# Performance work log

Hardware: AMD Instinct MI355X
Metric: run time of the kernel (lower is better)

## Reference

```python
import jax, jax.numpy as jnp
import numpy as np


def _mlp2(x, W1, b1, W2, b2):
    # ReluMLP with two Dense layers: relu between layers, linear output
    return jax.nn.relu(x @ W1 + b1) @ W2 + b2


def setup_inputs() -> dict:
    key = jax.random.key(0)
    N, NP, DIN, D = 100000, 25000, 16, 64
    E, EDS, EP, EUS = 1_600_000, 800_000, 400_000, 200_000
    L = 8  # number of message-passing layers actually used
    ks = iter(jax.random.split(key, 40))
    nrm = lambda shape: jax.random.normal(next(ks), shape, jnp.float32) * 0.05
    ri = lambda n, hi: jax.random.randint(next(ks), (n,), 0, hi)
    return dict(
        x=jax.random.normal(next(ks), (N, DIN), jnp.float32),
        We1=nrm((DIN, D)), be1=jnp.zeros((D,), jnp.float32),
        We2=nrm((D, D)), be2=jnp.zeros((D,), jnp.float32),
        Wm1=nrm((L, D, D)), bm1=jnp.zeros((L, D), jnp.float32),
        Wm2=nrm((L, D, D)), bm2=jnp.zeros((L, D), jnp.float32),
        Wn1=nrm((L, 2 * D, D)), bn1=jnp.zeros((L, D), jnp.float32),
        Wn2=nrm((L, D, D)), bn2=jnp.zeros((L, D), jnp.float32),
        Wd1=nrm((D, D)), bd1=jnp.zeros((D,), jnp.float32),
        Wd2=nrm((D, 2)), bd2=jnp.zeros((2,), jnp.float32),
        s_fine=ri(E, N), r_fine=ri(E, N),
        s_ds=ri(EDS, N), r_ds=ri(EDS, N),
        s_p=ri(EP, NP), r_p=ri(EP, NP),
        s_us=ri(EUS, NP), r_us=ri(EUS, NP),
        uppool=ri(N, NP), downpool=ri(NP, NP),
    )


def reference(x, We1, be1, We2, be2, Wm1, bm1, Wm2, bm2, Wn1, bn1, Wn2, bn2,
              Wd1, bd1, Wd2, bd2, s_fine, r_fine, s_ds, r_ds, s_p, r_p,
              s_us, r_us, uppool, downpool):
    def mp(l, h, s, r, n):
        # LinearMessagePassingLayer: message MLP on sender feats,
        # sum-scatter to receivers (mean_aggr=False), node MLP on [h, aggr]
        msg = _mlp2(h[s], Wm1[l], bm1[l], Wm2[l], bm2[l])          # [E, D]
        aggr = jax.ops.segment_sum(msg, r, num_segments=n)          # [n, D]
        return _mlp2(jnp.concatenate([h, aggr], -1),
                     Wn1[l], bn1[l], Wn2[l], bn2[l])                # [n, D]

    N = x.shape[0]
    NP = downpool.shape[0]
    # encode
    h = _mlp2(x, We1, be1, We2, be2)                                 # [N, D]
    h = mp(0, h, s_fine, r_fine, N)
    h = mp(1, h, s_fine, r_fine, N)
    skip = h
    # Downsample: gather by uppool idx, MP on downsampling graph, select pooled
    g = mp(2, h[uppool], s_ds, r_ds, N)                              # [N, D]
    hp = g[downpool]                                                 # [NP, D]
    # bottleneck
    hp = mp(3, hp, s_p, r_p, NP)
    hp = mp(4, hp, s_p, r_p, NP)
    # Upsample: gather by downpool idx, MP on upsampling graph, select by uppool
    g = mp(5, hp[downpool], s_us, r_us, NP)                          # [NP, D]
    h = g[uppool]                                                    # [N, D]
    # decode with skip connections
    h = mp(6, h, s_fine, r_fine, N) + skip
    h = mp(7, h, s_fine, r_fine, N) + skip
    return _mlp2(h, Wd1, bd1, Wd2, bd2)                              # [N, 2]
```

## Files before the change

kernel.cpp:

```cpp
#include <hip/hip_runtime.h>

#define WG 256

template<int DINA, bool HAS_B, bool HAS_SKIP, bool GATHER_A>
__global__ __launch_bounds__(WG)
void mlp2_rt(const float* __restrict__ inA, const int* __restrict__ gidxA,
             const float* __restrict__ inB,
             const float* __restrict__ W1, const float* __restrict__ b1,
             const float* __restrict__ W2, const float* __restrict__ b2,
             const float* __restrict__ skip,
             float* __restrict__ out, int n)
{
    constexpr int DIN = DINA + (HAS_B ? 64 : 0);
    constexpr int XROWS = (DIN > 64) ? DIN : 64;
    constexpr int XP = 68;
    __shared__ __align__(16) float sXT[XROWS][XP];
    __shared__ __align__(16) float sW[64 * 64];
    __shared__ float sb[128];

    const int tid = threadIdx.x;
    const int tx = tid & 15, ty = tid >> 4;
    const int c0 = tx * 4, r0 = ty * 4;
    const int row0 = blockIdx.x * 64;

    constexpr int K1 = (DIN > 64) ? 64 : DIN;
    for (int i = tid * 4; i < K1 * 64; i += WG * 4)
        *(float4*)&sW[i] = *(const float4*)&W1[i];
    if (tid < 64) sb[tid] = b1[tid];
    else if (tid < 128) sb[tid] = b2[tid - 64];

    {
        const int lrow = tid & 63;
        const int kq0 = (tid >> 6) * 4;
        const int rg = min(row0 + lrow, n - 1);
        const int ra = GATHER_A ? gidxA[rg] : rg;
        const float* pA = inA + (size_t)ra * DINA;
        #pragma unroll
        for (int kq = kq0; kq < DINA; kq += 16) {
            const float4 v = *(const float4*)(pA + kq);
            sXT[kq + 0][lrow] = v.x; sXT[kq + 1][lrow] = v.y;
            sXT[kq + 2][lrow] = v.z; sXT[kq + 3][lrow] = v.w;
        }
        if (HAS_B) {
            const float* pB = inB + (size_t)rg * 64;
            #pragma unroll
            for (int kq = kq0; kq < 64; kq += 16) {
                const float4 v = *(const float4*)(pB + kq);
                sXT[DINA + kq + 0][lrow] = v.x; sXT[DINA + kq + 1][lrow] = v.y;
                sXT[DINA + kq + 2][lrow] = v.z; sXT[DINA + kq + 3][lrow] = v.w;
            }
        }
    }
    __syncthreads();

    float acc[4][4] = {};
    #pragma unroll 8
    for (int k = 0; k < K1; ++k) {
        const float4 a = *(const float4*)&sXT[k][r0];
        const float4 w = *(const float4*)&sW[k * 64 + c0];
        acc[0][0] = fmaf(a.x, w.x, acc[0][0]); acc[0][1] = fmaf(a.x, w.y, acc[0][1]);
        acc[0][2] = fmaf(a.x, w.z, acc[0][2]); acc[0][3] = fmaf(a.x, w.w, acc[0][3]);
        acc[1][0] = fmaf(a.y, w.x, acc[1][0]); acc[1][1] = fmaf(a.y, w.y, acc[1][1]);
        acc[1][2] = fmaf(a.y, w.z, acc[1][2]); acc[1][3] = fmaf(a.y, w.w, acc[1][3]);
        acc[2][0] = fmaf(a.z, w.x, acc[2][0]); acc[2][1] = fmaf(a.z, w.y, acc[2][1]);
        acc[2][2] = fmaf(a.z, w.z, acc[2][2]); acc[2][3] = fmaf(a.z, w.w, acc[2][3]);
        acc[3][0] = fmaf(a.w, w.x, acc[3][0]); acc[3][1] = fmaf(a.w, w.y, acc[3][1]);
        acc[3][2] = fmaf(a.w, w.z, acc[3][2]); acc[3][3] = fmaf(a.w, w.w, acc[3][3]);
    }

    if constexpr (DIN > 64) {
        __syncthreads();
        for (int i = tid * 4; i < 64 * 64; i += WG * 4)
            *(float4*)&sW[i] = *(const float4*)&W1[64 * 64 + i];
        __syncthreads();
        #pragma unroll 8
        for (int kk = 0; kk < 64; ++kk) {
            const float4 a = *(const float4*)&sXT[64 + kk][r0];
            const float4 w = *(const float4*)&sW[kk * 64 + c0];
            acc[0][0] = fmaf(a.x, w.x, acc[0][0]); acc[0][1] = fmaf(a.x, w.y, acc[0][1]);
            acc[0][2] = fmaf(a.x, w.z, acc[0][2]); acc[0][3] = fmaf(a.x, w.w, acc[0][3]);
            acc[1][0] = fmaf(a.y, w.x, acc[1][0]); acc[1][1] = fmaf(a.y, w.y, acc[1][1]);
            acc[1][2] = fmaf(a.y, w.z, acc[1][2]); acc[1][3] = fmaf(a.y, w.w, acc[1][3]);
            acc[2][0] = fmaf(a.z, w.x, acc[2][0]); acc[2][1] = fmaf(a.z, w.y, acc[2][1]);
            acc[2][2] = fmaf(a.z, w.z, acc[2][2]); acc[2][3] = fmaf(a.z, w.w, acc[2][3]);
            acc[3][0] = fmaf(a.w, w.x, acc[3][0]); acc[3][1] = fmaf(a.w, w.y, acc[3][1]);
            acc[3][2] = fmaf(a.w, w.z, acc[3][2]); acc[3][3] = fmaf(a.w, w.w, acc[3][3]);
        }
    }
    __syncthreads();

    for (int i = tid * 4; i < 64 * 64; i += WG * 4)
        *(float4*)&sW[i] = *(const float4*)&W2[i];
    #pragma unroll
    for (int j = 0; j < 4; ++j) {
        const float bj = sb[c0 + j];
        float4 hv;
        hv.x = fmaxf(acc[0][j] + bj, 0.0f);
        hv.y = fmaxf(acc[1][j] + bj, 0.0f);
        hv.z = fmaxf(acc[2][j] + bj, 0.0f);
        hv.w = fmaxf(acc[3][j] + bj, 0.0f);
        *(float4*)&sXT[c0 + j][r0] = hv;
    }
    __syncthreads();

    float acc2[4][4] = {};
    #pragma unroll 8
    for (int k = 0; k < 64; ++k) {
        const float4 a = *(const float4*)&sXT[k][r0];
        const float4 w = *(const float4*)&sW[k * 64 + c0];
        acc2[0][0] = fmaf(a.x, w.x, acc2[0][0]); acc2[0][1] = fmaf(a.x, w.y, acc2[0][1]);
        acc2[0][2] = fmaf(a.x, w.z, acc2[0][2]); acc2[0][3] = fmaf(a.x, w.w, acc2[0][3]);
        acc2[1][0] = fmaf(a.y, w.x, acc2[1][0]); acc2[1][1] = fmaf(a.y, w.y, acc2[1][1]);
        acc2[1][2] = fmaf(a.y, w.z, acc2[1][2]); acc2[1][3] = fmaf(a.y, w.w, acc2[1][3]);
        acc2[2][0] = fmaf(a.z, w.x, acc2[2][0]); acc2[2][1] = fmaf(a.z, w.y, acc2[2][1]);
        acc2[2][2] = fmaf(a.z, w.z, acc2[2][2]); acc2[2][3] = fmaf(a.z, w.w, acc2[2][3]);
        acc2[3][0] = fmaf(a.w, w.x, acc2[3][0]); acc2[3][1] = fmaf(a.w, w.y, acc2[3][1]);
        acc2[3][2] = fmaf(a.w, w.z, acc2[3][2]); acc2[3][3] = fmaf(a.w, w.w, acc2[3][3]);
    }
    #pragma unroll
    for (int i = 0; i < 4; ++i) {
        const int row = row0 + r0 + i;
        if (row < n) {
            float4 o;
            o.x = acc2[i][0] + sb[64 + c0 + 0];
            o.y = acc2[i][1] + sb[64 + c0 + 1];
            o.z = acc2[i][2] + sb[64 + c0 + 2];
            o.w = acc2[i][3] + sb[64 + c0 + 3];
            if (HAS_SKIP) {
                const float4 s = *(const float4*)&skip[(size_t)row * 64 + c0];
                o.x += s.x; o.y += s.y; o.z += s.z; o.w += s.w;
            }
            *(float4*)&out[(size_t)row * 64 + c0] = o;
        }
    }
}

__global__ __launch_bounds__(WG)
void mlp2_rt_out2(const float* __restrict__ inA,
                  const float* __restrict__ W1, const float* __restrict__ b1,
                  const float* __restrict__ W2, const float* __restrict__ b2,
                  float* __restrict__ out, int n)
{
    constexpr int XP = 68;
    __shared__ __align__(16) float sXT[64][XP];
    __shared__ __align__(16) float sW[64 * 64];
    __shared__ float sb1[64];
    __shared__ float sW2[128];
    __shared__ float sb2[2];

    const int tid = threadIdx.x;
    const int tx = tid & 15, ty = tid >> 4;
    const int c0 = tx * 4, r0 = ty * 4;
    const int row0 = blockIdx.x * 64;

    for (int i = tid * 4; i < 64 * 64; i += WG * 4)
        *(float4*)&sW[i] = *(const float4*)&W1[i];
    if (tid < 64) sb1[tid] = b1[tid];
    else if (tid < 192) sW2[tid - 64] = W2[tid - 64];
    else if (tid < 194) sb2[tid - 192] = b2[tid - 192];

    {
        const int lrow = tid & 63;
        const int kq0 = (tid >> 6) * 4;
        const int rg = min(row0 + lrow, n - 1);
        const float* pA = inA + (size_t)rg * 64;
        #pragma unroll
        for (int kq = kq0; kq < 64; kq += 16) {
            const float4 v = *(const float4*)(pA + kq);
            sXT[kq + 0][lrow] = v.x; sXT[kq + 1][lrow] = v.y;
            sXT[kq + 2][lrow] = v.z; sXT[kq + 3][lrow] = v.w;
        }
    }
    __syncthreads();

    float acc[4][4] = {};
    #pragma unroll 8
    for (int k = 0; k < 64; ++k) {
        const float4 a = *(const float4*)&sXT[k][r0];
        const float4 w = *(const float4*)&sW[k * 64 + c0];
        acc[0][0] = fmaf(a.x, w.x, acc[0][0]); acc[0][1] = fmaf(a.x, w.y, acc[0][1]);
        acc[0][2] = fmaf(a.x, w.z, acc[0][2]); acc[0][3] = fmaf(a.x, w.w, acc[0][3]);
        acc[1][0] = fmaf(a.y, w.x, acc[1][0]); acc[1][1] = fmaf(a.y, w.y, acc[1][1]);
        acc[1][2] = fmaf(a.y, w.z, acc[1][2]); acc[1][3] = fmaf(a.y, w.w, acc[1][3]);
        acc[2][0] = fmaf(a.z, w.x, acc[2][0]); acc[2][1] = fmaf(a.z, w.y, acc[2][1]);
        acc[2][2] = fmaf(a.z, w.z, acc[2][2]); acc[2][3] = fmaf(a.z, w.w, acc[2][3]);
        acc[3][0] = fmaf(a.w, w.x, acc[3][0]); acc[3][1] = fmaf(a.w, w.y, acc[3][1]);
        acc[3][2] = fmaf(a.w, w.z, acc[3][2]); acc[3][3] = fmaf(a.w, w.w, acc[3][3]);
    }
    __syncthreads();
    #pragma unroll
    for (int j = 0; j < 4; ++j) {
        const float bj = sb1[c0 + j];
        float4 hv;
        hv.x = fmaxf(acc[0][j] + bj, 0.0f);
        hv.y = fmaxf(acc[1][j] + bj, 0.0f);
        hv.z = fmaxf(acc[2][j] + bj, 0.0f);
        hv.w = fmaxf(acc[3][j] + bj, 0.0f);
        *(float4*)&sXT[c0 + j][r0] = hv;
    }
    __syncthreads();

    if (tid < 128) {
        const int lr = tid >> 1, col = tid & 1;
        float o0 = sb2[col], o1 = 0.0f;
        #pragma unroll 8
        for (int k = 0; k < 64; k += 2) {
            o0 = fmaf(sXT[k][lr],     sW2[k * 2 + col],       o0);
            o1 = fmaf(sXT[k + 1][lr], sW2[(k + 1) * 2 + col], o1);
        }
        const int row = row0 + lr;
        if (row < n) out[(size_t)row * 2 + col] = o0 + o1;
    }
}

__global__ __launch_bounds__(WG)
void slot_fill_xcd_k(const int* __restrict__ s, const int* __restrict__ r,
                     int* __restrict__ cursor, int* __restrict__ slots,
                     int cap, int E, int n)
{
    const int xcd = blockIdx.x & 7;
    const int w   = blockIdx.x >> 3;
    const int W   = gridDim.x >> 3;
    const int lo  = (int)(((long)n * xcd) >> 3);
    const int hi  = (int)(((long)n * (xcd + 1)) >> 3);
    const int chunk = (E + W - 1) / W;
    const int e0 = w * chunk;
    const int e1 = min(E, e0 + chunk);
    for (int e = e0 + (int)threadIdx.x; e < e1; e += WG) {
        const int v = __builtin_nontemporal_load(&r[e]);
        if (v >= lo && v < hi) {
            const int sv = __builtin_nontemporal_load(&s[e]);
            const int p = atomicAdd(&cursor[v], 1);
            if (p < cap) slots[(size_t)v * cap + p] = sv;
        }
    }
}

template<bool REMAP>
__global__ __launch_bounds__(WG)
void gather_slots_k(const int* __restrict__ deg, const int* __restrict__ slots,
                    int cap, const int* __restrict__ remap,
                    const float* __restrict__ tab, float* __restrict__ aggr, int n)
{
    const int node = blockIdx.x * (WG / 64) + (threadIdx.x >> 6);
    const int c = threadIdx.x & 63;
    if (node >= n) return;
    const int d = min(deg[node], cap);
    const int* sl = slots + (size_t)node * cap;

    int myidx = 0;
    if (c < d) {
        myidx = __builtin_nontemporal_load(&sl[c]);
        if (REMAP) myidx = remap[myidx];
    }

    float a[8] = {};
    int j = 0;
    for (; j + 7 < d; j += 8) {
        #pragma unroll
        for (int u = 0; u < 8; ++u) {
            const int t = __shfl(myidx, j + u);
            a[u] += tab[(size_t)t * 64 + c];
        }
    }
    #pragma unroll 4
    for (; j < d; ++j) {
        const int t = __shfl(myidx, j);
        a[j & 7] += tab[(size_t)t * 64 + c];
    }
    const float v = ((a[0] + a[1]) + (a[2] + a[3])) + ((a[4] + a[5]) + (a[6] + a[7]));
    __builtin_nontemporal_store(v, &aggr[(size_t)node * 64 + c]);
}

extern "C" void kernel_launch(void* const* d_in, const int* in_sizes, int n_in,
                              void* d_out, int out_size, void* d_ws, size_t ws_size,
                              hipStream_t stream)
{
    const float* x    = (const float*)d_in[0];
    const float* We1  = (const float*)d_in[1];
    const float* be1  = (const float*)d_in[2];
    const float* We2  = (const float*)d_in[3];
    const float* be2  = (const float*)d_in[4];
    const float* Wm1  = (const float*)d_in[5];
    const float* bm1  = (const float*)d_in[6];
    const float* Wm2  = (const float*)d_in[7];
    const float* bm2  = (const float*)d_in[8];
    const float* Wn1  = (const float*)d_in[9];
    const float* bn1  = (const float*)d_in[10];
    const float* Wn2  = (const float*)d_in[11];
    const float* bn2  = (const float*)d_in[12];
    const float* Wd1  = (const float*)d_in[13];
    const float* bd1  = (const float*)d_in[14];
    const float* Wd2  = (const float*)d_in[15];
    const float* bd2  = (const float*)d_in[16];
    const int* s_fine = (const int*)d_in[17];
    const int* r_fine = (const int*)d_in[18];
    const int* s_ds   = (const int*)d_in[19];
    const int* r_ds   = (const int*)d_in[20];
    const int* s_p    = (const int*)d_in[21];
    const int* r_p    = (const int*)d_in[22];
    const int* s_us   = (const int*)d_in[23];
    const int* r_us   = (const int*)d_in[24];
    const int* uppool   = (const int*)d_in[25];
    const int* downpool = (const int*)d_in[26];

    const int N   = in_sizes[0] / 16;
    const int E   = in_sizes[17];
    const int EDS = in_sizes[19];
    const int EP  = in_sizes[21];
    const int EUS = in_sizes[23];
    const int NP  = in_sizes[26];

    const int CAP_FINE = 48;
    const int CAP_DS   = 32;
    const int CAP_PP   = 48;
    const int CAP_US   = 32;

    float* B0  = (float*)d_ws;
    float* B1  = B0 + (size_t)N * 64;
    float* B2  = B1 + (size_t)N * 64;
    float* B3  = B2 + (size_t)N * 64;
    float* HPa = B3 + (size_t)N * 64;
    float* HPb = HPa + (size_t)NP * 64;
    int* ip = (int*)(HPb + (size_t)NP * 64);
    auto alloc_i = [&](size_t n) { int* p = ip; ip += n; return p; };
    int* cur_fine = alloc_i(N);
    int* cur_ds   = alloc_i(N);
    int* cur_pp   = alloc_i(NP);
    int* cur_us   = alloc_i(NP);
    int* sl_fine  = alloc_i((size_t)N * CAP_FINE);
    int* sl_ds    = alloc_i((size_t)N * CAP_DS);
    int* sl_pp    = alloc_i((size_t)NP * CAP_PP);
    int* sl_us    = alloc_i((size_t)NP * CAP_US);

    const int gN  = (N + 63) / 64;
    const int gNP = (NP + 63) / 64;
    const int gaN  = (N + 3) / 4;
    const int gaNP = (NP + 3) / 4;

    hipMemsetAsync(cur_fine, 0, (size_t)(2 * N + 2 * NP) * sizeof(int), stream);
    slot_fill_xcd_k<<<2048, WG, 0, stream>>>(s_fine, r_fine, cur_fine, sl_fine, CAP_FINE, E,   N);
    slot_fill_xcd_k<<<1024, WG, 0, stream>>>(s_ds,   r_ds,   cur_ds,   sl_ds,   CAP_DS,   EDS, N);
    slot_fill_xcd_k<<<512,  WG, 0, stream>>>(s_p,    r_p,    cur_pp,   sl_pp,   CAP_PP,   EP,  NP);
    slot_fill_xcd_k<<<512,  WG, 0, stream>>>(s_us,   r_us,   cur_us,   sl_us,   CAP_US,   EUS, NP);

    mlp2_rt<16,false,false,false><<<gN,WG,0,stream>>>(x,nullptr,nullptr,We1,be1,We2,be2,nullptr,B0,N);

    mlp2_rt<64,false,false,false><<<gN,WG,0,stream>>>(B0,nullptr,nullptr,Wm1+0*4096,bm1+0*64,Wm2+0*4096,bm2+0*64,nullptr,B1,N);
    gather_slots_k<false><<<gaN,WG,0,stream>>>(cur_fine,sl_fine,CAP_FINE,nullptr,B1,B2,N);
    mlp2_rt<64,true,false,false><<<gN,WG,0,stream>>>(B0,nullptr,B2,Wn1+0*8192,bn1+0*64,Wn2+0*4096,bn2+0*64,nullptr,B3,N);

    mlp2_rt<64,false,false,false><<<gN,WG,0,stream>>>(B3,nullptr,nullptr,Wm1+1*4096,bm1+1*64,Wm2+1*4096,bm2+1*64,nullptr,B0,N);
    gather_slots_k<false><<<gaN,WG,0,stream>>>(cur_fine,sl_fine,CAP_FINE,nullptr,B0,B2,N);
    mlp2_rt<64,true,false,false><<<gN,WG,0,stream>>>(B3,nullptr,B2,Wn1+1*8192,bn1+1*64,Wn2+1*4096,bn2+1*64,nullptr,B1,N);

    mlp2_rt<64,false,false,false><<<gNP,WG,0,stream>>>(B1,nullptr,nullptr,Wm1+2*4096,bm1+2*64,Wm2+2*4096,bm2+2*64,nullptr,B0,NP);
    gather_slots_k<true><<<gaN,WG,0,stream>>>(cur_ds,sl_ds,CAP_DS,uppool,B0,B2,N);
    mlp2_rt<64,true,false,true><<<gN,WG,0,stream>>>(B1,uppool,B2,Wn1+2*8192,bn1+2*64,Wn2+2*4096,bn2+2*64,nullptr,B3,N);

    mlp2_rt<64,false,false,true><<<gNP,WG,0,stream>>>(B3,downpool,nullptr,Wm1+3*4096,bm1+3*64,Wm2+3*4096,bm2+3*64,nullptr,HPa,NP);
    gather_slots_k<false><<<gaNP,WG,0,stream>>>(cur_pp,sl_pp,CAP_PP,nullptr,HPa,B2,NP);
    mlp2_rt<64,true,false,true><<<gNP,WG,0,stream>>>(B3,downpool,B2,Wn1+3*8192,bn1+3*64,Wn2+3*4096,bn2+3*64,nullptr,HPb,NP);

    mlp2_rt<64,false,false,false><<<gNP,WG,0,stream>>>(HPb,nullptr,nullptr,Wm1+4*4096,bm1+4*64,Wm2+4*4096,bm2+4*64,nullptr,HPa,NP);
    gather_slots_k<false><<<gaNP,WG,0,stream>>>(cur_pp,sl_pp,CAP_PP,nullptr,HPa,B2,NP);
    mlp2_rt<64,true,false,false><<<gNP,WG,0,stream>>>(HPb,nullptr,B2,Wn1+4*8192,bn1+4*64,Wn2+4*4096,bn2+4*64,nullptr,HPa,NP);

    mlp2_rt<64,false,false,false><<<gNP,WG,0,stream>>>(HPa,nullptr,nullptr,Wm1+5*4096,bm1+5*64,Wm2+5*4096,bm2+5*64,nullptr,HPb,NP);
    gather_slots_k<true><<<gaNP,WG,0,stream>>>(cur_us,sl_us,CAP_US,downpool,HPb,B2,NP);
    mlp2_rt<64,true,false,true><<<gNP,WG,0,stream>>>(HPa,downpool,B2,Wn1+5*8192,bn1+5*64,Wn2+5*4096,bn2+5*64,nullptr,HPb,NP);

    mlp2_rt<64,false,false,false><<<gNP,WG,0,stream>>>(HPb,nullptr,nullptr,Wm1+6*4096,bm1+6*64,Wm2+6*4096,bm2+6*64,nullptr,HPa,NP);
    gather_slots_k<true><<<gaN,WG,0,stream>>>(cur_fine,sl_fine,CAP_FINE,uppool,HPa,B2,N);
    mlp2_rt<64,true,true,true><<<gN,WG,0,stream>>>(HPb,uppool,B2,Wn1+6*8192,bn1+6*64,Wn2+6*4096,bn2+6*64,B1,B0,N);

    mlp2_rt<64,false,false,false><<<gN,WG,0,stream>>>(B0,nullptr,nullptr,Wm1+7*4096,bm1+7*64,Wm2+7*4096,bm2+7*64,nullptr,B3,N);
    gather_slots_k<false><<<gaN,WG,0,stream>>>(cur_fine,sl_fine,CAP_FINE,nullptr,B3,B2,N);
    mlp2_rt<64,true,true,false><<<gN,WG,0,stream>>>(B0,nullptr,B2,Wn1+7*8192,bn1+7*64,Wn2+7*4096,bn2+7*64,B1,B3,N);

    mlp2_rt_out2<<<gN,WG,0,stream>>>(B3,Wd1,bd1,Wd2,bd2,(float*)d_out,N);
}
```

Before: 1.156 ms.

## Fuse each node MLP with the next layer's message MLP in one kernel

Adds a templated fused kernel that runs the node MLP of one layer and then, from the same on-chip tile, runs the message MLP of the next layer (or the final 64→2 decoder). Each fused launch writes both the node output and the per-node message. This removes a separate launch and a global re-read of the node features for most layers. It also replaces the nontemporal store in the gather kernel with a plain store. The cost is more shared-memory reloads per block and longer kernels, and some outputs are computed in place on the same buffer, which relies on each row being read and written only by its own block.

```diff
diff --git a/kernel.cpp b/kernel.cpp
--- a/kernel.cpp
+++ b/kernel.cpp
@@ -1,6 +1,206 @@
 #include <hip/hip_runtime.h>
 
 #define WG 256
+
+#define MLP_FMA16(ACC, A, W) do { \
+    ACC[0][0]=fmaf(A.x,W.x,ACC[0][0]); ACC[0][1]=fmaf(A.x,W.y,ACC[0][1]); \
+    ACC[0][2]=fmaf(A.x,W.z,ACC[0][2]); ACC[0][3]=fmaf(A.x,W.w,ACC[0][3]); \
+    ACC[1][0]=fmaf(A.y,W.x,ACC[1][0]); ACC[1][1]=fmaf(A.y,W.y,ACC[1][1]); \
+    ACC[1][2]=fmaf(A.y,W.z,ACC[1][2]); ACC[1][3]=fmaf(A.y,W.w,ACC[1][3]); \
+    ACC[2][0]=fmaf(A.z,W.x,ACC[2][0]); ACC[2][1]=fmaf(A.z,W.y,ACC[2][1]); \
+    ACC[2][2]=fmaf(A.z,W.z,ACC[2][2]); ACC[2][3]=fmaf(A.z,W.w,ACC[2][3]); \
+    ACC[3][0]=fmaf(A.w,W.x,ACC[3][0]); ACC[3][1]=fmaf(A.w,W.y,ACC[3][1]); \
+    ACC[3][2]=fmaf(A.w,W.z,ACC[3][2]); ACC[3][3]=fmaf(A.w,W.w,ACC[3][3]); \
+} while (0)
+
+template<int DINA, bool HAS_B, bool HAS_SKIP, bool GATHER_A,
+         int MSG_DOUT, bool PARTIAL_MSG, bool WRITE_OUT1>
+__global__ __launch_bounds__(WG)
+void mlp2_fused(const float* __restrict__ inA, const int* __restrict__ gidxA,
+                const float* __restrict__ inB,
+                const float* __restrict__ W1, const float* __restrict__ b1,
+                const float* __restrict__ W2, const float* __restrict__ b2,
+                const float* __restrict__ skip, float* __restrict__ out1,
+                const float* __restrict__ M1, const float* __restrict__ mb1,
+                const float* __restrict__ M2, const float* __restrict__ mb2,
+                float* __restrict__ outM, int msgN, int n)
+{
+    constexpr int DIN = DINA + (HAS_B ? 64 : 0);
+    constexpr int XROWS = (DIN > 64) ? DIN : 64;
+    constexpr int XP = 68;
+    __shared__ __align__(16) float sXT[XROWS][XP];
+    __shared__ __align__(16) float sW[64 * 64];
+    __shared__ float sb[128];
+    __shared__ float sW2d[128];
+    __shared__ float sb2d[2];
+
+    const int tid = threadIdx.x;
+    const int tx = tid & 15, ty = tid >> 4;
+    const int c0 = tx * 4, r0 = ty * 4;
+    const int row0 = blockIdx.x * 64;
+
+    constexpr int K1 = (DIN > 64) ? 64 : DIN;
+    for (int i = tid * 4; i < K1 * 64; i += WG * 4)
+        *(float4*)&sW[i] = *(const float4*)&W1[i];
+    if (tid < 64) sb[tid] = b1[tid];
+    else if (tid < 128) sb[tid] = b2[tid - 64];
+
+    {
+        const int lrow = tid & 63;
+        const int kq0 = (tid >> 6) * 4;
+        const int rg = min(row0 + lrow, n - 1);
+        const int ra = GATHER_A ? gidxA[rg] : rg;
+        const float* pA = inA + (size_t)ra * DINA;
+        #pragma unroll
+        for (int kq = kq0; kq < DINA; kq += 16) {
+            const float4 v = *(const float4*)(pA + kq);
+            sXT[kq + 0][lrow] = v.x; sXT[kq + 1][lrow] = v.y;
+            sXT[kq + 2][lrow] = v.z; sXT[kq + 3][lrow] = v.w;
+        }
+        if (HAS_B) {
+            const float* pB = inB + (size_t)rg * 64;
+            #pragma unroll
+            for (int kq = kq0; kq < 64; kq += 16) {
+                const float4 v = *(const float4*)(pB + kq);
+                sXT[DINA + kq + 0][lrow] = v.x; sXT[DINA + kq + 1][lrow] = v.y;
+                sXT[DINA + kq + 2][lrow] = v.z; sXT[DINA + kq + 3][lrow] = v.w;
+            }
+        }
+    }
+    __syncthreads();
+
+    float acc[4][4] = {};
+    #pragma unroll 8
+    for (int k = 0; k < K1; ++k) {
+        const float4 a = *(const float4*)&sXT[k][r0];
+        const float4 w = *(const float4*)&sW[k * 64 + c0];
+        MLP_FMA16(acc, a, w);
+    }
+    if constexpr (DIN > 64) {
+        __syncthreads();
+        for (int i = tid * 4; i < 64 * 64; i += WG * 4)
+            *(float4*)&sW[i] = *(const float4*)&W1[64 * 64 + i];
+        __syncthreads();
+        #pragma unroll 8
+        for (int kk = 0; kk < 64; ++kk) {
+            const float4 a = *(const float4*)&sXT[64 + kk][r0];
+            const float4 w = *(const float4*)&sW[kk * 64 + c0];
+            MLP_FMA16(acc, a, w);
+        }
+    }
+    __syncthreads();
+
+    for (int i = tid * 4; i < 64 * 64; i += WG * 4)
+        *(float4*)&sW[i] = *(const float4*)&W2[i];
+    #pragma unroll
+    for (int j = 0; j < 4; ++j) {
+        const float bj = sb[c0 + j];
+        float4 hv = make_float4(fmaxf(acc[0][j] + bj, 0.0f),
+                                fmaxf(acc[1][j] + bj, 0.0f),
+                                fmaxf(acc[2][j] + bj, 0.0f),
+                                fmaxf(acc[3][j] + bj, 0.0f));
+        *(float4*)&sXT[c0 + j][r0] = hv;
+    }
+    __syncthreads();
+
+    float acc2[4][4] = {};
+    #pragma unroll 8
+    for (int k = 0; k < 64; ++k) {
+        const float4 a = *(const float4*)&sXT[k][r0];
+        const float4 w = *(const float4*)&sW[k * 64 + c0];
+        MLP_FMA16(acc2, a, w);
+    }
+
+    float ofull[4][4];
+    #pragma unroll
+    for (int i = 0; i < 4; ++i) {
+        const int row = row0 + r0 + i;
+        float4 s = make_float4(0.f, 0.f, 0.f, 0.f);
+        if (HAS_SKIP && row < n) s = *(const float4*)&skip[(size_t)row * 64 + c0];
+        ofull[i][0] = acc2[i][0] + sb[64 + c0 + 0] + s.x;
+        ofull[i][1] = acc2[i][1] + sb[64 + c0 + 1] + s.y;
+        ofull[i][2] = acc2[i][2] + sb[64 + c0 + 2] + s.z;
+        ofull[i][3] = acc2[i][3] + sb[64 + c0 + 3] + s.w;
+        if (WRITE_OUT1 && row < n)
+            *(float4*)&out1[(size_t)row * 64 + c0] =
+                make_float4(ofull[i][0], ofull[i][1], ofull[i][2], ofull[i][3]);
+    }
+
+    if constexpr (MSG_DOUT > 0) {
+        if (!PARTIAL_MSG || row0 < msgN) {
+            __syncthreads();
+            for (int i = tid * 4; i < 64 * 64; i += WG * 4)
+                *(float4*)&sW[i] = *(const float4*)&M1[i];
+            if (tid < 64) sb[tid] = mb1[tid];
+            if constexpr (MSG_DOUT == 64) {
+                if (tid >= 64 && tid < 128) sb[tid] = mb2[tid - 64];
+            } else {
+                if (tid >= 64 && tid < 192) sW2d[tid - 64] = M2[tid - 64];
+                if (tid >= 192 && tid < 194) sb2d[tid - 192] = mb2[tid - 192];
+            }
+            #pragma unroll
+            for (int j = 0; j < 4; ++j)
+                *(float4*)&sXT[c0 + j][r0] =
+                    make_float4(ofull[0][j], ofull[1][j], ofull[2][j], ofull[3][j]);
+            __syncthreads();
+
+            float acc3[4][4] = {};
+            #pragma unroll 8
+            for (int k = 0; k < 64; ++k) {
+                const float4 a = *(const float4*)&sXT[k][r0];
+                const float4 w = *(const float4*)&sW[k * 64 + c0];
+                MLP_FMA16(acc3, a, w);
+            }
+            __syncthreads();
+            if constexpr (MSG_DOUT == 64) {
+                for (int i = tid * 4; i < 64 * 64; i += WG * 4)
+                    *(float4*)&sW[i] = *(const float4*)&M2[i];
+            }
+            #pragma unroll
+            for (int j = 0; j < 4; ++j) {
+                const float bj = sb[c0 + j];
+                float4 hv = make_float4(fmaxf(acc3[0][j] + bj, 0.0f),
+                                        fmaxf(acc3[1][j] + bj, 0.0f),
+                                        fmaxf(acc3[2][j] + bj, 0.0f),
+                                        fmaxf(acc3[3][j] + bj, 0.0f));
+                *(float4*)&sXT[c0 + j][r0] = hv;
+            }
+            __syncthreads();
+
+            if constexpr (MSG_DOUT == 64) {
+                float accM[4][4] = {};
+                #pragma unroll 8
+                for (int k = 0; k < 64; ++k) {
+                    const float4 a = *(const float4*)&sXT[k][r0];
+                    const float4 w = *(const float4*)&sW[k * 64 + c0];
+                    MLP_FMA16(accM, a, w);
+                }
+                #pragma unroll
+                for (int i = 0; i < 4; ++i) {
+                    const int row = row0 + r0 + i;
+                    if (row < msgN)
+                        *(float4*)&outM[(size_t)row * 64 + c0] =
+                            make_float4(accM[i][0] + sb[64 + c0 + 0],
+                                        accM[i][1] + sb[64 + c0 + 1],
+                                        accM[i][2] + sb[64 + c0 + 2],
+                                        accM[i][3] + sb[64 + c0 + 3]);
+                }
+            } else {
+                if (tid < 128) {
+                    const int lr = tid >> 1, col = tid & 1;
+                    float o0 = sb2d[col], o1 = 0.0f;
+                    #pragma unroll 8
+                    for (int k = 0; k < 64; k += 2) {
+                        o0 = fmaf(sXT[k][lr],     sW2d[k * 2 + col],       o0);
+                        o1 = fmaf(sXT[k + 1][lr], sW2d[(k + 1) * 2 + col], o1);
+                    }
+                    const int row = row0 + lr;
+                    if (row < msgN) outM[(size_t)row * 2 + col] = o0 + o1;
+                }
+            }
+        }
+    }
+}
 
 template<int DINA, bool HAS_B, bool HAS_SKIP, bool GATHER_A>
 __global__ __launch_bounds__(WG)
@@ -58,16 +258,8 @@
     for (int k = 0; k < K1; ++k) {
         const float4 a = *(const float4*)&sXT[k][r0];
         const float4 w = *(const float4*)&sW[k * 64 + c0];
-        acc[0][0] = fmaf(a.x, w.x, acc[0][0]); acc[0][1] = fmaf(a.x, w.y, acc[0][1]);
-        acc[0][2] = fmaf(a.x, w.z, acc[0][2]); acc[0][3] = fmaf(a.x, w.w, acc[0][3]);
-        acc[1][0] = fmaf(a.y, w.x, acc[1][0]); acc[1][1] = fmaf(a.y, w.y, acc[1][1]);
-        acc[1][2] = fmaf(a.y, w.z, acc[1][2]); acc[1][3] = fmaf(a.y, w.w, acc[1][3]);
-        acc[2][0] = fmaf(a.z, w.x, acc[2][0]); acc[2][1] = fmaf(a.z, w.y, acc[2][1]);
-        acc[2][2] = fmaf(a.z, w.z, acc[2][2]); acc[2][3] = fmaf(a.z, w.w, acc[2][3]);
-        acc[3][0] = fmaf(a.w, w.x, acc[3][0]); acc[3][1] = fmaf(a.w, w.y, acc[3][1]);
-        acc[3][2] = fmaf(a.w, w.z, acc[3][2]); acc[3][3] = fmaf(a.w, w.w, acc[3][3]);
-    }
-
+        MLP_FMA16(acc, a, w);
+    }
     if constexpr (DIN > 64) {
         __syncthreads();
         for (int i = tid * 4; i < 64 * 64; i += WG * 4)
@@ -77,14 +269,7 @@
         for (int kk = 0; kk < 64; ++kk) {
             const float4 a = *(const float4*)&sXT[64 + kk][r0];
             const float4 w = *(const float4*)&sW[kk * 64 + c0];
-            acc[0][0] = fmaf(a.x, w.x, acc[0][0]); acc[0][1] = fmaf(a.x, w.y, acc[0][1]);
-            acc[0][2] = fmaf(a.x, w.z, acc[0][2]); acc[0][3] = fmaf(a.x, w.w, acc[0][3]);
-            acc[1][0] = fmaf(a.y, w.x, acc[1][0]); acc[1][1] = fmaf(a.y, w.y, acc[1][1]);
-            acc[1][2] = fmaf(a.y, w.z, acc[1][2]); acc[1][3] = fmaf(a.y, w.w, acc[1][3]);
-            acc[2][0] = fmaf(a.z, w.x, acc[2][0]); acc[2][1] = fmaf(a.z, w.y, acc[2][1]);
-            acc[2][2] = fmaf(a.z, w.z, acc[2][2]); acc[2][3] = fmaf(a.z, w.w, acc[2][3]);
-            acc[3][0] = fmaf(a.w, w.x, acc[3][0]); acc[3][1] = fmaf(a.w, w.y, acc[3][1]);
-            acc[3][2] = fmaf(a.w, w.z, acc[3][2]); acc[3][3] = fmaf(a.w, w.w, acc[3][3]);
+            MLP_FMA16(acc, a, w);
         }
     }
     __syncthreads();
@@ -94,11 +279,10 @@
     #pragma unroll
     for (int j = 0; j < 4; ++j) {
         const float bj = sb[c0 + j];
-        float4 hv;
-        hv.x = fmaxf(acc[0][j] + bj, 0.0f);
-        hv.y = fmaxf(acc[1][j] + bj, 0.0f);
-        hv.z = fmaxf(acc[2][j] + bj, 0.0f);
-        hv.w = fmaxf(acc[3][j] + bj, 0.0f);
+        float4 hv = make_float4(fmaxf(acc[0][j] + bj, 0.0f),
+                                fmaxf(acc[1][j] + bj, 0.0f),
+                                fmaxf(acc[2][j] + bj, 0.0f),
+                                fmaxf(acc[3][j] + bj, 0.0f));
         *(float4*)&sXT[c0 + j][r0] = hv;
     }
     __syncthreads();
@@ -108,108 +292,22 @@
     for (int k = 0; k < 64; ++k) {
         const float4 a = *(const float4*)&sXT[k][r0];
         const float4 w = *(const float4*)&sW[k * 64 + c0];
-        acc2[0][0] = fmaf(a.x, w.x, acc2[0][0]); acc2[0][1] = fmaf(a.x, w.y, acc2[0][1]);
-        acc2[0][2] = fmaf(a.x, w.z, acc2[0][2]); acc2[0][3] = fmaf(a.x, w.w, acc2[0][3]);
-        acc2[1][0] = fmaf(a.y, w.x, acc2[1][0]); acc2[1][1] = fmaf(a.y, w.y, acc2[1][1]);
-        acc2[1][2] = fmaf(a.y, w.z, acc2[1][2]); acc2[1][3] = fmaf(a.y, w.w, acc2[1][3]);
-        acc2[2][0] = fmaf(a.z, w.x, acc2[2][0]); acc2[2][1] = fmaf(a.z, w.y, acc2[2][1]);
-        acc2[2][2] = fmaf(a.z, w.z, acc2[2][2]); acc2[2][3] = fmaf(a.z, w.w, acc2[2][3]);
-        acc2[3][0] = fmaf(a.w, w.x, acc2[3][0]); acc2[3][1] = fmaf(a.w, w.y, acc2[3][1]);
-        acc2[3][2] = fmaf(a.w, w.z, acc2[3][2]); acc2[3][3] = fmaf(a.w, w.w, acc2[3][3]);
+        MLP_FMA16(acc2, a, w);
     }
     #pragma unroll
     for (int i = 0; i < 4; ++i) {
         const int row = row0 + r0 + i;
         if (row < n) {
-            float4 o;
-            o.x = acc2[i][0] + sb[64 + c0 + 0];
-            o.y = acc2[i][1] + sb[64 + c0 + 1];
-            o.z = acc2[i][2] + sb[64 + c0 + 2];
-            o.w = acc2[i][3] + sb[64 + c0 + 3];
+            float4 o = make_float4(acc2[i][0] + sb[64 + c0 + 0],
+                                   acc2[i][1] + sb[64 + c0 + 1],
+                                   acc2[i][2] + sb[64 + c0 + 2],
+                                   acc2[i][3] + sb[64 + c0 + 3]);
             if (HAS_SKIP) {
                 const float4 s = *(const float4*)&skip[(size_t)row * 64 + c0];
                 o.x += s.x; o.y += s.y; o.z += s.z; o.w += s.w;
             }
             *(float4*)&out[(size_t)row * 64 + c0] = o;
         }
-    }
-}
-
-__global__ __launch_bounds__(WG)
-void mlp2_rt_out2(const float* __restrict__ inA,
-                  const float* __restrict__ W1, const float* __restrict__ b1,
-                  const float* __restrict__ W2, const float* __restrict__ b2,
-                  float* __restrict__ out, int n)
-{
-    constexpr int XP = 68;
-    __shared__ __align__(16) float sXT[64][XP];
-    __shared__ __align__(16) float sW[64 * 64];
-    __shared__ float sb1[64];
-    __shared__ float sW2[128];
-    __shared__ float sb2[2];
-
-    const int tid = threadIdx.x;
-    const int tx = tid & 15, ty = tid >> 4;
-    const int c0 = tx * 4, r0 = ty * 4;
-    const int row0 = blockIdx.x * 64;
-
-    for (int i = tid * 4; i < 64 * 64; i += WG * 4)
-        *(float4*)&sW[i] = *(const float4*)&W1[i];
-    if (tid < 64) sb1[tid] = b1[tid];
-    else if (tid < 192) sW2[tid - 64] = W2[tid - 64];
-    else if (tid < 194) sb2[tid - 192] = b2[tid - 192];
-
-    {
-        const int lrow = tid & 63;
-        const int kq0 = (tid >> 6) * 4;
-        const int rg = min(row0 + lrow, n - 1);
-        const float* pA = inA + (size_t)rg * 64;
-        #pragma unroll
-        for (int kq = kq0; kq < 64; kq += 16) {
-            const float4 v = *(const float4*)(pA + kq);
-            sXT[kq + 0][lrow] = v.x; sXT[kq + 1][lrow] = v.y;
-            sXT[kq + 2][lrow] = v.z; sXT[kq + 3][lrow] = v.w;
-        }
-    }
-    __syncthreads();
-
-    float acc[4][4] = {};
-    #pragma unroll 8
-    for (int k = 0; k < 64; ++k) {
-        const float4 a = *(const float4*)&sXT[k][r0];
-        const float4 w = *(const float4*)&sW[k * 64 + c0];
-        acc[0][0] = fmaf(a.x, w.x, acc[0][0]); acc[0][1] = fmaf(a.x, w.y, acc[0][1]);
-        acc[0][2] = fmaf(a.x, w.z, acc[0][2]); acc[0][3] = fmaf(a.x, w.w, acc[0][3]);
-        acc[1][0] = fmaf(a.y, w.x, acc[1][0]); acc[1][1] = fmaf(a.y, w.y, acc[1][1]);
-        acc[1][2] = fmaf(a.y, w.z, acc[1][2]); acc[1][3] = fmaf(a.y, w.w, acc[1][3]);
-        acc[2][0] = fmaf(a.z, w.x, acc[2][0]); acc[2][1] = fmaf(a.z, w.y, acc[2][1]);
-        acc[2][2] = fmaf(a.z, w.z, acc[2][2]); acc[2][3] = fmaf(a.z, w.w, acc[2][3]);
-        acc[3][0] = fmaf(a.w, w.x, acc[3][0]); acc[3][1] = fmaf(a.w, w.y, acc[3][1]);
-        acc[3][2] = fmaf(a.w, w.z, acc[3][2]); acc[3][3] = fmaf(a.w, w.w, acc[3][3]);
-    }
-    __syncthreads();
-    #pragma unroll
-    for (int j = 0; j < 4; ++j) {
-        const float bj = sb1[c0 + j];
-        float4 hv;
-        hv.x = fmaxf(acc[0][j] + bj, 0.0f);
-        hv.y = fmaxf(acc[1][j] + bj, 0.0f);
-        hv.z = fmaxf(acc[2][j] + bj, 0.0f);
-        hv.w = fmaxf(acc[3][j] + bj, 0.0f);
-        *(float4*)&sXT[c0 + j][r0] = hv;
-    }
-    __syncthreads();
-
-    if (tid < 128) {
-        const int lr = tid >> 1, col = tid & 1;
-        float o0 = sb2[col], o1 = 0.0f;
-        #pragma unroll 8
-        for (int k = 0; k < 64; k += 2) {
-            o0 = fmaf(sXT[k][lr],     sW2[k * 2 + col],       o0);
-            o1 = fmaf(sXT[k + 1][lr], sW2[(k + 1) * 2 + col], o1);
-        }
-        const int row = row0 + lr;
-        if (row < n) out[(size_t)row * 2 + col] = o0 + o1;
     }
 }
 
@@ -268,8 +366,8 @@
         const int t = __shfl(myidx, j);
         a[j & 7] += tab[(size_t)t * 64 + c];
     }
-    const float v = ((a[0] + a[1]) + (a[2] + a[3])) + ((a[4] + a[5]) + (a[6] + a[7]));
-    __builtin_nontemporal_store(v, &aggr[(size_t)node * 64 + c]);
+    aggr[(size_t)node * 64 + c] =
+        ((a[0] + a[1]) + (a[2] + a[3])) + ((a[4] + a[5]) + (a[6] + a[7]));
 }
 
 extern "C" void kernel_launch(void* const* d_in, const int* in_sizes, int n_in,
@@ -311,10 +409,7 @@
     const int EUS = in_sizes[23];
     const int NP  = in_sizes[26];
 
-    const int CAP_FINE = 48;
-    const int CAP_DS   = 32;
-    const int CAP_PP   = 48;
-    const int CAP_US   = 32;
+    const int CAP_FINE = 48, CAP_DS = 32, CAP_PP = 48, CAP_US = 32;
 
     float* B0  = (float*)d_ws;
     float* B1  = B0 + (size_t)N * 64;
@@ -344,39 +439,49 @@
     slot_fill_xcd_k<<<512,  WG, 0, stream>>>(s_p,    r_p,    cur_pp,   sl_pp,   CAP_PP,   EP,  NP);
     slot_fill_xcd_k<<<512,  WG, 0, stream>>>(s_us,   r_us,   cur_us,   sl_us,   CAP_US,   EUS, NP);
 
-    mlp2_rt<16,false,false,false><<<gN,WG,0,stream>>>(x,nullptr,nullptr,We1,be1,We2,be2,nullptr,B0,N);
-
-    mlp2_rt<64,false,false,false><<<gN,WG,0,stream>>>(B0,nullptr,nullptr,Wm1+0*4096,bm1+0*64,Wm2+0*4096,bm2+0*64,nullptr,B1,N);
+    mlp2_fused<16,false,false,false,64,false,true><<<gN,WG,0,stream>>>(
+        x,nullptr,nullptr, We1,be1,We2,be2, nullptr,B0,
+        Wm1+0*4096,bm1+0*64,Wm2+0*4096,bm2+0*64, B1, N, N);
     gather_slots_k<false><<<gaN,WG,0,stream>>>(cur_fine,sl_fine,CAP_FINE,nullptr,B1,B2,N);
-    mlp2_rt<64,true,false,false><<<gN,WG,0,stream>>>(B0,nullptr,B2,Wn1+0*8192,bn1+0*64,Wn2+0*4096,bn2+0*64,nullptr,B3,N);
-
-    mlp2_rt<64,false,false,false><<<gN,WG,0,stream>>>(B3,nullptr,nullptr,Wm1+1*4096,bm1+1*64,Wm2+1*4096,bm2+1*64,nullptr,B0,N);
+
+    mlp2_fused<64,true,false,false,64,false,true><<<gN,WG,0,stream>>>(
+        B0,nullptr,B2, Wn1+0*8192,bn1+0*64,Wn2+0*4096,bn2+0*64, nullptr,B3,
+        Wm1+1*4096,bm1+1*64,Wm2+1*4096,bm2+1*64, B0, N, N);
     gather_slots_k<false><<<gaN,WG,0,stream>>>(cur_fine,sl_fine,CAP_FINE,nullptr,B0,B2,N);
-    mlp2_rt<64,true,false,false><<<gN,WG,0,stream>>>(B3,nullptr,B2,Wn1+1*8192,bn1+1*64,Wn2+1*4096,bn2+1*64,nullptr,B1,N);
-
-    mlp2_rt<64,false,false,false><<<gNP,WG,0,stream>>>(B1,nullptr,nullptr,Wm1+2*4096,bm1+2*64,Wm2+2*4096,bm2+2*64,nullptr,B0,NP);
+
+    mlp2_fused<64,true,false,false,64,true,true><<<gN,WG,0,stream>>>(
+        B3,nullptr,B2, Wn1+1*8192,bn1+1*64,Wn2+1*4096,bn2+1*64, nullptr,B1,
+        Wm1+2*4096,bm1+2*64,Wm2+2*4096,bm2+2*64, B0, NP, N);
     gather_slots_k<true><<<gaN,WG,0,stream>>>(cur_ds,sl_ds,CAP_DS,uppool,B0,B2,N);
-    mlp2_rt<64,true,false,true><<<gN,WG,0,stream>>>(B1,uppool,B2,Wn1+2*8192,bn1+2*64,Wn2+2*4096,bn2+2*64,nullptr,B3,N);
-
-    mlp2_rt<64,false,false,true><<<gNP,WG,0,stream>>>(B3,downpool,nullptr,Wm1+3*4096,bm1+3*64,Wm2+3*4096,bm2+3*64,nullptr,HPa,NP);
+
+    mlp2_rt<64,true,false,true><<<gN,WG,0,stream>>>(
+        B1,uppool,B2, Wn1+2*8192,bn1+2*64,Wn2+2*4096,bn2+2*64, nullptr,B3,N);
+
+    mlp2_rt<64,false,false,true><<<gNP,WG,0,stream>>>(
+        B3,downpool,nullptr, Wm1+3*4096,bm1+3*64,Wm2+3*4096,bm2+3*64, nullptr,HPa,NP);
     gather_slots_k<false><<<gaNP,WG,0,stream>>>(cur_pp,sl_pp,CAP_PP,nullptr,HPa,B2,NP);
-    mlp2_rt<64,true,false,true><<<gNP,WG,0,stream>>>(B3,downpool,B2,Wn1+3*8192,bn1+3*64,Wn2+3*4096,bn2+3*64,nullptr,HPb,NP);
-
-    mlp2_rt<64,false,false,false><<<gNP,WG,0,stream>>>(HPb,nullptr,nullptr,Wm1+4*4096,bm1+4*64,Wm2+4*4096,bm2+4*64,nullptr,HPa,NP);
+
+    mlp2_fused<64,true,false,true,64,false,true><<<gNP,WG,0,stream>>>(
+        B3,downpool,B2, Wn1+3*8192,bn1+3*64,Wn2+3*4096,bn2+3*64, nullptr,HPb,
+        Wm1+4*4096,bm1+4*64,Wm2+4*4096,bm2+4*64, HPa, NP, NP);
     gather_slots_k<false><<<gaNP,WG,0,stream>>>(cur_pp,sl_pp,CAP_PP,nullptr,HPa,B2,NP);
-    mlp2_rt<64,true,false,false><<<gNP,WG,0,stream>>>(HPb,nullptr,B2,Wn1+4*8192,bn1+4*64,Wn2+4*4096,bn2+4*64,nullptr,HPa,NP);
-
-    mlp2_rt<64,false,false,false><<<gNP,WG,0,stream>>>(HPa,nullptr,nullptr,Wm1+5*4096,bm1+5*64,Wm2+5*4096,bm2+5*64,nullptr,HPb,NP);
+
+    mlp2_fused<64,true,false,false,64,false,true><<<gNP,WG,0,stream>>>(
+        HPb,nullptr,B2, Wn1+4*8192,bn1+4*64,Wn2+4*4096,bn2+4*64, nullptr,HPa,
+        Wm1+5*4096,bm1+5*64,Wm2+5*4096,bm2+5*64, HPb, NP, NP);
     gather_slots_k<true><<<gaNP,WG,0,stream>>>(cur_us,sl_us,CAP_US,downpool,HPb,B2,NP);
-    mlp2_rt<64,true,false,true><<<gNP,WG,0,stream>>>(HPa,downpool,B2,Wn1+5*8192,bn1+5*64,Wn2+5*4096,bn2+5*64,nullptr,HPb,NP);
-
-    mlp2_rt<64,false,false,false><<<gNP,WG,0,stream>>>(HPb,nullptr,nullptr,Wm1+6*4096,bm1+6*64,Wm2+6*4096,bm2+6*64,nullptr,HPa,NP);
-    gather_slots_k<true><<<gaN,WG,0,stream>>>(cur_fine,sl_fine,CAP_FINE,uppool,HPa,B2,N);
-    mlp2_rt<64,true,true,true><<<gN,WG,0,stream>>>(HPb,uppool,B2,Wn1+6*8192,bn1+6*64,Wn2+6*4096,bn2+6*64,B1,B0,N);
-
-    mlp2_rt<64,false,false,false><<<gN,WG,0,stream>>>(B0,nullptr,nullptr,Wm1+7*4096,bm1+7*64,Wm2+7*4096,bm2+7*64,nullptr,B3,N);
+
+    mlp2_fused<64,true,false,true,64,false,true><<<gNP,WG,0,stream>>>(
+        HPa,downpool,B2, Wn1+5*8192,bn1+5*64,Wn2+5*4096,bn2+5*64, nullptr,HPb,
+        Wm1+6*4096,bm1+6*64,Wm2+6*4096,bm2+6*64, B3, NP, NP);
+    gather_slots_k<true><<<gaN,WG,0,stream>>>(cur_fine,sl_fine,CAP_FINE,uppool,B3,B2,N);
+
+    mlp2_fused<64,true,true,true,64,false,true><<<gN,WG,0,stream>>>(
+        HPb,uppool,B2, Wn1+6*8192,bn1+6*64,Wn2+6*4096,bn2+6*64, B1,B0,
+        Wm1+7*4096,bm1+7*64,Wm2+7*4096,bm2+7*64, B3, N, N);
     gather_slots_k<false><<<gaN,WG,0,stream>>>(cur_fine,sl_fine,CAP_FINE,nullptr,B3,B2,N);
-    mlp2_rt<64,true,true,false><<<gN,WG,0,stream>>>(B0,nullptr,B2,Wn1+7*8192,bn1+7*64,Wn2+7*4096,bn2+7*64,B1,B3,N);
-
-    mlp2_rt_out2<<<gN,WG,0,stream>>>(B3,Wd1,bd1,Wd2,bd2,(float*)d_out,N);
+
+    mlp2_fused<64,true,true,false,2,false,false><<<gN,WG,0,stream>>>(
+        B0,nullptr,B2, Wn1+7*8192,bn1+7*64,Wn2+7*4096,bn2+7*64, B1,nullptr,
+        Wd1,bd1,Wd2,bd2, (float*)d_out, N, N);
 }
```

New measurement: 1.091 ms. -5.6%, faster.
